# Optimization experiments

Measured on AMD Instinct MI355X. Metric: run time of the kernel, lower is better.

## Reference

```python
import jax, jax.numpy as jnp
import numpy as np


def reference(x, y, max_disp):
    # x, y: [B, C, H, W] left/right feature maps (stride-3 features)
    # Builds cost[b, :C, i, h, w]  = x[b, :, h, w]      for w >= i else 0
    #        cost[b, C:, i, h, w] = y[b, :, h, w - i]  for w >= i else 0
    # i.e. the vectorized form of the original Python loop over disparities.
    D = max_disp // 3
    B, C, H, W = x.shape
    d = jnp.arange(D)
    w = jnp.arange(W)
    mask = (w[None, :] >= d[:, None]).astype(x.dtype)          # [D, W]
    m = mask[None, None, :, None, :]                            # [1,1,D,1,W]
    cost_x = x[:, :, None, :, :] * m                            # [B,C,D,H,W]
    idx = jnp.clip(w[None, :] - d[:, None], 0, W - 1)           # [D, W]
    y_shift = y[:, :, :, idx]                                   # [B,C,H,D,W]
    cost_y = jnp.transpose(y_shift, (0, 1, 3, 2, 4)) * m        # [B,C,D,H,W]
    return jnp.concatenate([cost_x, cost_y], axis=1)            # [B,2C,D,H,W]


def setup_inputs() -> dict:
    key = jax.random.key(0)
    k1, k2 = jax.random.split(key)
    B, C, H, W = 1, 32, 96, 192
    x = jax.random.normal(k1, (B, C, H, W), dtype=jnp.float32)
    y = jax.random.normal(k2, (B, C, H, W), dtype=jnp.float32)
    return {"x": x, "y": y, "max_disp": 192}
```

## Files before the change

### kernel.cpp

```cpp
#include <hip/hip_runtime.h>

constexpr int C      = 32;
constexpr int D      = 64;
constexpr int H      = 96;
constexpr int W      = 192;
constexpr int PLANE4 = H * W / 4;
constexpr int TOTAL4 = 2 * C * D * PLANE4;

typedef float f4  __attribute__((ext_vector_type(4)));
typedef float f4u __attribute__((ext_vector_type(4), aligned(4)));

__global__ __launch_bounds__(256) void fusion_kernel(const float* __restrict__ x,
                                                     const float* __restrict__ y,
                                                     float* __restrict__ out) {
    const int nthreads = gridDim.x * blockDim.x;
    int o4 = blockIdx.x * blockDim.x + threadIdx.x;
    #pragma unroll 2
    for (; o4 < TOTAL4; o4 += nthreads) {
        const int chd = o4 / PLANE4;
        const int rem = o4 - chd * PLANE4;
        const int ch  = chd >> 6;
        const int d   = chd & 63;
        const int w   = (rem % 48) * 4;

        f4 v;
        if (ch < C) {
            v = *(const f4*)(x + ch * (H * W) + rem * 4);
        } else {
            const int off = (ch - C) * (H * W) + rem * 4 - d;
            if (off >= 0) {
                v = *(const f4u*)(y + off);
            } else {
                v.x = y[max(off + 0, 0)];
                v.y = y[max(off + 1, 0)];
                v.z = y[max(off + 2, 0)];
                v.w = y[max(off + 3, 0)];
            }
        }
        if (w < d) {
            if (w + 0 < d) v.x = 0.f;
            if (w + 1 < d) v.y = 0.f;
            if (w + 2 < d) v.z = 0.f;
            if (w + 3 < d) v.w = 0.f;
        }
        *(f4*)(out + (long long)o4 * 4) = v;
    }
}

extern "C" void kernel_launch(void* const* d_in, const int* in_sizes, int n_in,
                              void* d_out, int out_size, void* d_ws, size_t ws_size,
                              hipStream_t stream) {
    const float* x = (const float*)d_in[0];
    const float* y = (const float*)d_in[1];
    float* out     = (float*)d_out;

    constexpr int block = 256;
    constexpr int grid  = 4608;
    fusion_kernel<<<grid, block, 0, stream>>>(x, y, out);
}
```

Before: 322.1 us.

## Give each thread a fixed column strip of 16 rows with batched loads

Replaces the grid-stride loop with a one-shot mapping in which each thread owns one 4-wide column across 16 consecutive rows of a (channel, disparity) plane. Per-element index division and mask computation are hoisted out, and the 16 loads are issued before the 16 stores to raise memory-level parallelism. The cost is 16 float4 values held in registers per thread and a grid sized exactly to the fixed problem shape. The kernel is a pure write-bound broadcast, so any change in speed should come mainly from store and load scheduling.

```diff
diff --git a/kernel.cpp b/kernel.cpp
--- a/kernel.cpp
+++ b/kernel.cpp
@@ -1,11 +1,12 @@
 #include <hip/hip_runtime.h>
 
-constexpr int C      = 32;
-constexpr int D      = 64;
-constexpr int H      = 96;
-constexpr int W      = 192;
-constexpr int PLANE4 = H * W / 4;
-constexpr int TOTAL4 = 2 * C * D * PLANE4;
+constexpr int C     = 32;
+constexpr int D     = 64;
+constexpr int H     = 96;
+constexpr int W     = 192;
+constexpr int W4    = W / 4;
+constexpr int HB    = 6;
+constexpr int HITER = 16;
 
 typedef float f4  __attribute__((ext_vector_type(4)));
 typedef float f4u __attribute__((ext_vector_type(4), aligned(4)));
@@ -13,37 +14,53 @@
 __global__ __launch_bounds__(256) void fusion_kernel(const float* __restrict__ x,
                                                      const float* __restrict__ y,
                                                      float* __restrict__ out) {
-    const int nthreads = gridDim.x * blockDim.x;
-    int o4 = blockIdx.x * blockDim.x + threadIdx.x;
-    #pragma unroll 2
-    for (; o4 < TOTAL4; o4 += nthreads) {
-        const int chd = o4 / PLANE4;
-        const int rem = o4 - chd * PLANE4;
-        const int ch  = chd >> 6;
-        const int d   = chd & 63;
-        const int w   = (rem % 48) * 4;
+    const int tid = blockIdx.x * blockDim.x + threadIdx.x;
+    const int w4  = tid % W4;
+    int rest      = tid / W4;
+    const int hb  = rest % HB;
+    rest         /= HB;
+    const int d   = rest % D;
+    const int ch  = rest / D;
+    const int w   = w4 * 4;
+    const int h0  = hb * HITER;
 
-        f4 v;
-        if (ch < C) {
-            v = *(const f4*)(x + ch * (H * W) + rem * 4);
+    const int outoff = (ch * D + d) * (H * W) + h0 * W + w;
+
+    const bool m0 = (w + 0) < d;
+    const bool m1 = (w + 1) < d;
+    const bool m2 = (w + 2) < d;
+    const bool m3 = (w + 3) < d;
+
+    f4 v[HITER];
+
+    if (ch < C) {
+        const float* xr = x + ch * (H * W) + h0 * W + w;
+        #pragma unroll
+        for (int i = 0; i < HITER; ++i)
+            v[i] = *(const f4*)(xr + i * W);
+    } else {
+        const int off0 = (ch - C) * (H * W) + h0 * W + w - d;
+        if (off0 >= 0) {
+            v[0] = *(const f4u*)(y + off0);
         } else {
-            const int off = (ch - C) * (H * W) + rem * 4 - d;
-            if (off >= 0) {
-                v = *(const f4u*)(y + off);
-            } else {
-                v.x = y[max(off + 0, 0)];
-                v.y = y[max(off + 1, 0)];
-                v.z = y[max(off + 2, 0)];
-                v.w = y[max(off + 3, 0)];
-            }
+            v[0].x = y[max(off0 + 0, 0)];
+            v[0].y = y[max(off0 + 1, 0)];
+            v[0].z = y[max(off0 + 2, 0)];
+            v[0].w = y[max(off0 + 3, 0)];
         }
-        if (w < d) {
-            if (w + 0 < d) v.x = 0.f;
-            if (w + 1 < d) v.y = 0.f;
-            if (w + 2 < d) v.z = 0.f;
-            if (w + 3 < d) v.w = 0.f;
-        }
-        *(f4*)(out + (long long)o4 * 4) = v;
+        #pragma unroll
+        for (int i = 1; i < HITER; ++i)
+            v[i] = *(const f4u*)(y + off0 + i * W);
+    }
+
+    #pragma unroll
+    for (int i = 0; i < HITER; ++i) {
+        f4 s = v[i];
+        if (m0) s.x = 0.f;
+        if (m1) s.y = 0.f;
+        if (m2) s.z = 0.f;
+        if (m3) s.w = 0.f;
+        *(f4*)(out + outoff + i * W) = s;
     }
 }
 
@@ -54,7 +71,8 @@
     const float* y = (const float*)d_in[1];
     float* out     = (float*)d_out;
 
+    constexpr int total = 2 * C * D * HB * W4;
     constexpr int block = 256;
-    constexpr int grid  = 4608;
+    constexpr int grid  = total / block;
     fusion_kernel<<<grid, block, 0, stream>>>(x, y, out);
 }
```

Result: faster. 311.4 us (-3.3%).
